# Performance work log

Hardware: AMD Instinct MI355X
Metric: run time of the kernel (lower is better)

Reference implementation:

```python
import jax, jax.numpy as jnp
import numpy as np

EPS = 1e-5


def setup_inputs() -> dict:
    key = jax.random.key(0)
    ks = jax.random.split(key, 8)
    g, p, d, h, w = 32, 64, 512, 24, 8
    hw = h * w
    return {
        "gal_fea": jax.random.normal(ks[0], (g, d, h, w), dtype=jnp.float32),
        "prob_fea": jax.random.normal(ks[1], (p, d, h, w), dtype=jnp.float32),
        "bn_weight": jnp.ones((1,), jnp.float32),
        "bn_bias": jnp.zeros((1,), jnp.float32),
        "bn_mean": jax.random.normal(ks[2], (1,), jnp.float32) * 0.1,
        "bn_var": jax.random.uniform(ks[3], (1,), jnp.float32, 0.5, 1.5),
        "fc_weight": jax.random.normal(ks[4], (1, 2 * hw), jnp.float32) * 0.05,
        "fc_bias": jnp.zeros((1,), jnp.float32),
        "lbn_weight": jnp.ones((1,), jnp.float32),
        "lbn_bias": jnp.zeros((1,), jnp.float32),
        "lbn_mean": jax.random.normal(ks[5], (1,), jnp.float32) * 0.1,
        "lbn_var": jax.random.uniform(ks[6], (1,), jnp.float32, 0.5, 1.5),
    }


def reference(gal_fea, prob_fea, bn_weight, bn_bias, bn_mean, bn_var,
              fc_weight, fc_bias, lbn_weight, lbn_bias, lbn_mean, lbn_var):
    g, d, h, w = gal_fea.shape
    p = prob_fea.shape[0]
    hw = h * w
    # 1x1 conv with probe pixels as kernels == batched correlation (QK^T style)
    gal = gal_fea.reshape(g, d, hw)                                  # [g, d, hw_x]
    ker = jnp.transpose(prob_fea, (0, 2, 3, 1)).reshape(p, hw, d)    # [p, hw_y, d]
    s = jnp.einsum('gdx,pyd->gpyx', gal, ker)                        # [g, p, hw_y, hw_x]
    # dual-axis max pooling, then concat: [g, p, 2*hw]
    score = jnp.concatenate([s.max(axis=2), s.max(axis=3)], axis=-1)
    # BatchNorm1d(1) in eval mode: scalar affine with running stats
    score = (score - bn_mean) * (bn_weight / jnp.sqrt(bn_var + EPS)) + bn_bias
    # fc: Linear(2*hw, 1)
    score = score.reshape(g * p, 2 * hw) @ fc_weight[0] + fc_bias[0]  # [g*p]
    score = score.reshape(g, p)
    # logit BatchNorm1d(1), eval mode
    score = (score - lbn_mean) * (lbn_weight / jnp.sqrt(lbn_var + EPS)) + lbn_bias
    return jax.nn.sigmoid(score / 10.0)
```

## Files before the change

kernel.cpp:

```cpp
#include <hip/hip_runtime.h>
#include <hip/hip_bf16.h>
#include <cstdint>
#include <cstddef>

#define NG 32
#define NP 64
#define ND 512
#define HW 192
#define EPSV 1e-5f

typedef _Float16 half8 __attribute__((ext_vector_type(8)));
typedef float floatx4 __attribute__((ext_vector_type(4)));
typedef float floatx16 __attribute__((ext_vector_type(16)));

__global__ __launch_bounds__(192) void prep_probe(const float* __restrict__ prob,
                                                  _Float16* __restrict__ probT2) {
  const int p = blockIdx.x, s = blockIdx.y;
  const int r = threadIdx.x;
  const float* src = prob + ((size_t)p * ND + s * 8) * HW + r;
  half8 h;
#pragma unroll
  for (int j = 0; j < 8; ++j) h[j] = (_Float16)src[(size_t)j * HW];
  *(half8*)(probT2 + (((size_t)p * 64 + s) * HW + r) * 8) = h;
}

__global__ __launch_bounds__(256) void prep_gal(const float* __restrict__ gal,
                                                _Float16* __restrict__ galT) {
  __shared__ float tile[32][33];
  const int zg = blockIdx.z;
  const float* sp = gal + (size_t)zg * ND * HW;
  _Float16* dp = galT + (size_t)zg * HW * ND;
  const int k0 = blockIdx.x * 32, s0 = blockIdx.y * 32;
  const int tx = threadIdx.x & 31, ty = threadIdx.x >> 5;
#pragma unroll
  for (int i = ty; i < 32; i += 8)
    tile[i][tx] = sp[(size_t)(k0 + i) * HW + s0 + tx];
  __syncthreads();
#pragma unroll
  for (int i = ty; i < 32; i += 8)
    dp[(size_t)(s0 + i) * ND + k0 + tx] = (_Float16)tile[tx][i];
}

__device__ __forceinline__ void g2l16(const void* g, void* l) {
  __builtin_amdgcn_global_load_lds(
      (const __attribute__((address_space(1))) void*)g,
      (__attribute__((address_space(3))) void*)l, 16, 0, 0);
}

__global__ __launch_bounds__(256, 2) void qaconv_main(
    const _Float16* __restrict__ galT, const _Float16* __restrict__ probT2,
    const float* __restrict__ bn_w, const float* __restrict__ bn_b,
    const float* __restrict__ bn_m, const float* __restrict__ bn_v,
    const float* __restrict__ fc_w, const float* __restrict__ fc_b,
    const float* __restrict__ lbn_w, const float* __restrict__ lbn_b,
    const float* __restrict__ lbn_m, const float* __restrict__ lbn_v,
    float* __restrict__ out) {
  __shared__ __align__(16) char shmem[50688];
  __shared__ float colp[2][HW];
  __shared__ float wsum[4];
  char* bufB = shmem;
  float(*rowbuf)[66] = (float(*)[66])shmem;

  const int bid = blockIdx.x;
  const int g = bid >> 6, p = bid & 63;

  const int t = threadIdx.x;
  const int lane = t & 63, wid = t >> 6;
  const int wr = wid & 1;
  const int wc = wid >> 1;
  const int l31 = lane & 31, hi = lane >> 5;
  const int arow0 = wr * 96 + l31;

  const _Float16* aBase = probT2 + (((size_t)p * 64 + hi) * HW + arow0) * 8;

  const _Float16* gBl = galT + (size_t)g * HW * ND + (size_t)(t & 31) * ND + ((t >> 5) & 7) * 8;
  const int sdst = wid * 1024;

  floatx16 acc[3][3];
#pragma unroll
  for (int ii = 0; ii < 3; ++ii)
#pragma unroll
    for (int jj = 0; jj < 3; ++jj) acc[ii][jj] = (floatx16)0.f;

#define STAGE_B(kt_, buf_)                                          \
  {                                                                 \
    char* db_ = bufB + (buf_)*24576 + sdst;                         \
    const _Float16* sb_ = gBl + (size_t)(kt_)*64;                   \
    _Pragma("unroll") for (int r_ = 0; r_ < 6; ++r_)                \
        g2l16(sb_ + (size_t)r_ * 32 * ND, db_ + r_ * 4096);         \
  }

#define LOAD_AF(dst, idx_)                                          \
  {                                                                 \
    const _Float16* ap_ = aBase + (size_t)(idx_) * (2 * HW * 8);    \
    dst[0] = *(const half8*)(ap_);                                  \
    dst[1] = *(const half8*)(ap_ + 32 * 8);                         \
    dst[2] = *(const half8*)(ap_ + 64 * 8);                         \
  }

#define KC_BODY(kc_, AFU, AFL, nidx_)                                            \
  {                                                                              \
    LOAD_AF(AFL, nidx_);                                                         \
    half8 bf[3];                                                                 \
    const int boff_ = ((kc_)*2 + hi) * 512 + l31 * 16;                           \
    bf[0] = *(const half8*)(bcur + (wc * 3 + 0) * 4096 + boff_);                 \
    bf[1] = *(const half8*)(bcur + (wc * 3 + 1) * 4096 + boff_);                 \
    bf[2] = *(const half8*)(bcur + (wc * 3 + 2) * 4096 + boff_);                 \
    __builtin_amdgcn_s_setprio(1);                                               \
    _Pragma("unroll") for (int ii = 0; ii < 3; ++ii)                             \
        _Pragma("unroll") for (int jj = 0; jj < 3; ++jj)                         \
            acc[ii][jj] = __builtin_amdgcn_mfma_f32_32x32x16_f16(AFU[ii], bf[jj],\
                                                                 acc[ii][jj], 0, 0, 0); \
    __builtin_amdgcn_s_setprio(0);                                               \
  }

  half8 af0[3], af1[3];
  STAGE_B(0, 0);
  LOAD_AF(af0, 0);
  __syncthreads();

  for (int kt = 0; kt < 8; ++kt) {
    if (kt < 7) STAGE_B(kt + 1, (kt & 1) ^ 1);
    const char* bcur = bufB + (kt & 1) * 24576;
    const int i0 = kt * 4;
    const int n4 = (kt < 7) ? i0 + 4 : 31;
    KC_BODY(0, af0, af1, i0 + 1)
    KC_BODY(1, af1, af0, i0 + 2)
    KC_BODY(2, af0, af1, i0 + 3)
    KC_BODY(3, af1, af0, n4)
    __syncthreads();
  }

#pragma unroll
  for (int fb = 0; fb < 3; ++fb) {
    float v = -3.4e38f;
#pragma unroll
    for (int fa = 0; fa < 3; ++fa)
#pragma unroll
      for (int e = 0; e < 16; ++e) v = fmaxf(v, acc[fa][fb][e]);
    v = fmaxf(v, __shfl_xor(v, 32));
    if (lane < 32) colp[wr][wc * 96 + fb * 32 + lane] = v;
  }
#pragma unroll
  for (int fa = 0; fa < 3; ++fa)
#pragma unroll
    for (int e = 0; e < 16; ++e) {
      float rv = acc[fa][0][e];
      rv = fmaxf(rv, acc[fa][1][e]);
      rv = fmaxf(rv, acc[fa][2][e]);
      const int Y = wr * 96 + fa * 32 + (e & 3) + 8 * (e >> 2) + 4 * hi;
      rowbuf[Y][wc * 32 + l31] = rv;
    }
  __syncthreads();

  float partial = 0.f;
  if (t < HW) {
    const float* rb = rowbuf[t];
    float rmax = -3.4e38f;
#pragma unroll
    for (int j = 0; j < 16; ++j) {
      const floatx4 v = *(const floatx4*)&rb[j * 4];
      rmax = fmaxf(rmax, fmaxf(fmaxf(v[0], v[1]), fmaxf(v[2], v[3])));
    }
    const float cmax = fmaxf(colp[0][t], colp[1][t]);
    const float scale = bn_w[0] / sqrtf(bn_v[0] + EPSV);
    const float bm = bn_m[0], bb = bn_b[0];
    partial = ((cmax - bm) * scale + bb) * fc_w[t] +
              ((rmax - bm) * scale + bb) * fc_w[HW + t];
  }
#pragma unroll
  for (int off = 1; off < 64; off <<= 1) partial += __shfl_xor(partial, off);
  if (lane == 0) wsum[wid] = partial;
  __syncthreads();
  if (t == 0) {
    const float sum = fc_b[0] + wsum[0] + wsum[1] + wsum[2] + wsum[3];
    const float logit = (sum - lbn_m[0]) * (lbn_w[0] / sqrtf(lbn_v[0] + EPSV)) + lbn_b[0];
    out[bid] = 1.f / (1.f + expf(-logit * 0.1f));
  }
#undef STAGE_B
#undef LOAD_AF
#undef KC_BODY
}

__global__ __launch_bounds__(256) void qaconv_naive(
    const float* __restrict__ gal, const float* __restrict__ prob,
    const float* __restrict__ bn_w, const float* __restrict__ bn_b,
    const float* __restrict__ bn_m, const float* __restrict__ bn_v,
    const float* __restrict__ fc_w, const float* __restrict__ fc_b,
    const float* __restrict__ lbn_w, const float* __restrict__ lbn_b,
    const float* __restrict__ lbn_m, const float* __restrict__ lbn_v,
    float* __restrict__ out) {
  __shared__ float prow[ND];
  __shared__ float rowmaxs[HW];
  __shared__ float colmaxs[HW];
  __shared__ float red[4];
  const int bid = blockIdx.x;
  const int g = bid >> 6, p = bid & 63;
  const int t = threadIdx.x, lane = t & 63, wid = t >> 6;
  const float* gp = gal + (size_t)g * ND * HW;
  const float* pp = prob + (size_t)p * ND * HW;
  float colmax = -3.4e38f;
  for (int y = 0; y < HW; ++y) {
    for (int k = t; k < ND; k += 256) prow[k] = pp[(size_t)k * HW + y];
    __syncthreads();
    float sv = -3.4e38f;
    if (t < HW) {
      sv = 0.f;
      for (int k = 0; k < ND; ++k) sv = fmaf(prow[k], gp[(size_t)k * HW + t], sv);
      colmax = fmaxf(colmax, sv);
    }
    float m = sv;
#pragma unroll
    for (int off = 1; off < 64; off <<= 1) m = fmaxf(m, __shfl_xor(m, off));
    if (lane == 0) red[wid] = m;
    __syncthreads();
    if (t == 0) rowmaxs[y] = fmaxf(fmaxf(red[0], red[1]), fmaxf(red[2], red[3]));
    __syncthreads();
  }
  if (t < HW) colmaxs[t] = colmax;
  __syncthreads();
  float partial = 0.f;
  for (int j = t; j < 2 * HW; j += 256) {
    const float v = (j < HW) ? colmaxs[j] : rowmaxs[j - HW];
    const float sc = (v - bn_m[0]) * (bn_w[0] / sqrtf(bn_v[0] + EPSV)) + bn_b[0];
    partial += sc * fc_w[j];
  }
#pragma unroll
  for (int off = 1; off < 64; off <<= 1) partial += __shfl_xor(partial, off);
  if (lane == 0) red[wid] = partial;
  __syncthreads();
  if (t == 0) {
    const float sum = fc_b[0] + red[0] + red[1] + red[2] + red[3];
    const float logit = (sum - lbn_m[0]) * (lbn_w[0] / sqrtf(lbn_v[0] + EPSV)) + lbn_b[0];
    out[bid] = 1.f / (1.f + expf(-logit * 0.1f));
  }
}

extern "C" void kernel_launch(void* const* d_in, const int* in_sizes, int n_in,
                              void* d_out, int out_size, void* d_ws, size_t ws_size,
                              hipStream_t stream) {
  const float* gal = (const float*)d_in[0];
  const float* prob = (const float*)d_in[1];
  const float* bn_w = (const float*)d_in[2];
  const float* bn_b = (const float*)d_in[3];
  const float* bn_m = (const float*)d_in[4];
  const float* bn_v = (const float*)d_in[5];
  const float* fc_w = (const float*)d_in[6];
  const float* fc_b = (const float*)d_in[7];
  const float* lbn_w = (const float*)d_in[8];
  const float* lbn_b = (const float*)d_in[9];
  const float* lbn_m = (const float*)d_in[10];
  const float* lbn_v = (const float*)d_in[11];
  float* out = (float*)d_out;

  const size_t probT2_elems = (size_t)NP * 64 * HW * 8;
  const size_t galT_elems = (size_t)NG * HW * ND;
  const size_t ws_needed = (probT2_elems + galT_elems) * sizeof(_Float16);
  if (ws_size >= ws_needed) {
    _Float16* probT2 = (_Float16*)d_ws;
    _Float16* galT = probT2 + probT2_elems;
    prep_probe<<<dim3(NP, 64), dim3(192), 0, stream>>>(prob, probT2);
    prep_gal<<<dim3(16, 6, NG), dim3(256), 0, stream>>>(gal, galT);
    qaconv_main<<<dim3(NG * NP), dim3(256), 0, stream>>>(
        galT, probT2, bn_w, bn_b, bn_m, bn_v, fc_w, fc_b, lbn_w, lbn_b, lbn_m, lbn_v, out);
  } else {
    qaconv_naive<<<dim3(NG * NP), dim3(256), 0, stream>>>(
        gal, prob, bn_w, bn_b, bn_m, bn_v, fc_w, fc_b, lbn_w, lbn_b, lbn_m, lbn_v, out);
  }
}
```

Baseline: 108.5 us.

## Pre-tile both operands in MFMA fragment order and stage both through LDS

```diff
diff --git a/kernel.cpp b/kernel.cpp
--- a/kernel.cpp
+++ b/kernel.cpp
@@ -7,38 +7,41 @@
 #define NP 64
 #define ND 512
 #define HW 192
+#define KT2 16
 #define EPSV 1e-5f
 
 typedef _Float16 half8 __attribute__((ext_vector_type(8)));
 typedef float floatx4 __attribute__((ext_vector_type(4)));
 typedef float floatx16 __attribute__((ext_vector_type(16)));
 
-__global__ __launch_bounds__(192) void prep_probe(const float* __restrict__ prob,
-                                                  _Float16* __restrict__ probT2) {
-  const int p = blockIdx.x, s = blockIdx.y;
-  const int r = threadIdx.x;
-  const float* src = prob + ((size_t)p * ND + s * 8) * HW + r;
-  half8 h;
-#pragma unroll
-  for (int j = 0; j < 8; ++j) h[j] = (_Float16)src[(size_t)j * HW];
-  *(half8*)(probT2 + (((size_t)p * 64 + s) * HW + r) * 8) = h;
-}
-
-__global__ __launch_bounds__(256) void prep_gal(const float* __restrict__ gal,
-                                                _Float16* __restrict__ galT) {
-  __shared__ float tile[32][33];
-  const int zg = blockIdx.z;
-  const float* sp = gal + (size_t)zg * ND * HW;
-  _Float16* dp = galT + (size_t)zg * HW * ND;
-  const int k0 = blockIdx.x * 32, s0 = blockIdx.y * 32;
-  const int tx = threadIdx.x & 31, ty = threadIdx.x >> 5;
-#pragma unroll
-  for (int i = ty; i < 32; i += 8)
-    tile[i][tx] = sp[(size_t)(k0 + i) * HW + s0 + tx];
-  __syncthreads();
-#pragma unroll
-  for (int i = ty; i < 32; i += 8)
-    dp[(size_t)(s0 + i) * ND + k0 + tx] = (_Float16)tile[tx][i];
+__global__ __launch_bounds__(256) void prep_tiles(const float* __restrict__ gal,
+                                                  const float* __restrict__ prob,
+                                                  _Float16* __restrict__ galT3,
+                                                  _Float16* __restrict__ probT3) {
+  const int z = blockIdx.x;
+  const int kt2 = blockIdx.y;
+  const float* src;
+  _Float16* dst;
+  if (z < NP) {
+    src = prob + (size_t)z * ND * HW;
+    dst = probT3 + (size_t)z * KT2 * 6144;
+  } else {
+    src = gal + (size_t)(z - NP) * ND * HW;
+    dst = galT3 + (size_t)(z - NP) * KT2 * 6144;
+  }
+  src += (size_t)kt2 * 32 * HW;
+  dst += (size_t)kt2 * 6144;
+  const int t = threadIdx.x;
+#pragma unroll
+  for (int r = 0; r < 3; ++r) {
+    const int h = r * 256 + t;
+    const int rb = h >> 7, kc = (h >> 6) & 1, hi = (h >> 5) & 1, l31 = h & 31;
+    const float* sp = src + (size_t)(kc * 16 + hi * 8) * HW + rb * 32 + l31;
+    half8 v;
+#pragma unroll
+    for (int j = 0; j < 8; ++j) v[j] = (_Float16)sp[(size_t)j * HW];
+    *(half8*)(dst + (size_t)h * 8) = v;
+  }
 }
 
 __device__ __forceinline__ void g2l16(const void* g, void* l) {
@@ -48,7 +51,7 @@
 }
 
 __global__ __launch_bounds__(256, 2) void qaconv_main(
-    const _Float16* __restrict__ galT, const _Float16* __restrict__ probT2,
+    const _Float16* __restrict__ galT3, const _Float16* __restrict__ probT3,
     const float* __restrict__ bn_w, const float* __restrict__ bn_b,
     const float* __restrict__ bn_m, const float* __restrict__ bn_v,
     const float* __restrict__ fc_w, const float* __restrict__ fc_b,
@@ -58,7 +61,7 @@
   __shared__ __align__(16) char shmem[50688];
   __shared__ float colp[2][HW];
   __shared__ float wsum[4];
-  char* bufB = shmem;
+  char* bufs = shmem;
   float(*rowbuf)[66] = (float(*)[66])shmem;
 
   const int bid = blockIdx.x;
@@ -69,11 +72,9 @@
   const int wr = wid & 1;
   const int wc = wid >> 1;
   const int l31 = lane & 31, hi = lane >> 5;
-  const int arow0 = wr * 96 + l31;
-
-  const _Float16* aBase = probT2 + (((size_t)p * 64 + hi) * HW + arow0) * 8;
-
-  const _Float16* gBl = galT + (size_t)g * HW * ND + (size_t)(t & 31) * ND + ((t >> 5) & 7) * 8;
+
+  const _Float16* pAl = probT3 + (size_t)p * KT2 * 6144 + wid * 512 + lane * 8;
+  const _Float16* pBl = galT3 + (size_t)g * KT2 * 6144 + wid * 512 + lane * 8;
   const int sdst = wid * 1024;
 
   floatx16 acc[3][3];
@@ -82,52 +83,44 @@
 #pragma unroll
     for (int jj = 0; jj < 3; ++jj) acc[ii][jj] = (floatx16)0.f;
 
-#define STAGE_B(kt_, buf_)                                          \
-  {                                                                 \
-    char* db_ = bufB + (buf_)*24576 + sdst;                         \
-    const _Float16* sb_ = gBl + (size_t)(kt_)*64;                   \
-    _Pragma("unroll") for (int r_ = 0; r_ < 6; ++r_)                \
-        g2l16(sb_ + (size_t)r_ * 32 * ND, db_ + r_ * 4096);         \
-  }
-
-#define LOAD_AF(dst, idx_)                                          \
-  {                                                                 \
-    const _Float16* ap_ = aBase + (size_t)(idx_) * (2 * HW * 8);    \
-    dst[0] = *(const half8*)(ap_);                                  \
-    dst[1] = *(const half8*)(ap_ + 32 * 8);                         \
-    dst[2] = *(const half8*)(ap_ + 64 * 8);                         \
-  }
-
-#define KC_BODY(kc_, AFU, AFL, nidx_)                                            \
+#define STAGE(kt_, b_)                                               \
+  {                                                                  \
+    char* db_ = bufs + (b_)*24576 + sdst;                            \
+    const _Float16* sa_ = pAl + (size_t)(kt_)*6144;                  \
+    const _Float16* sb_ = pBl + (size_t)(kt_)*6144;                  \
+    _Pragma("unroll") for (int r_ = 0; r_ < 3; ++r_)                 \
+        g2l16(sa_ + (size_t)r_ * 2048, db_ + r_ * 4096);             \
+    _Pragma("unroll") for (int r_ = 0; r_ < 3; ++r_)                 \
+        g2l16(sb_ + (size_t)r_ * 2048, db_ + 12288 + r_ * 4096);     \
+  }
+
+#define KC_BODY(kc_)                                                             \
   {                                                                              \
-    LOAD_AF(AFL, nidx_);                                                         \
-    half8 bf[3];                                                                 \
-    const int boff_ = ((kc_)*2 + hi) * 512 + l31 * 16;                           \
-    bf[0] = *(const half8*)(bcur + (wc * 3 + 0) * 4096 + boff_);                 \
-    bf[1] = *(const half8*)(bcur + (wc * 3 + 1) * 4096 + boff_);                 \
-    bf[2] = *(const half8*)(bcur + (wc * 3 + 2) * 4096 + boff_);                 \
+    half8 af[3], bf[3];                                                          \
+    const int off_ = (kc_)*1024 + hi * 512 + l31 * 16;                           \
+    af[0] = *(const half8*)(bA + (wr * 3 + 0) * 2048 + off_);                    \
+    af[1] = *(const half8*)(bA + (wr * 3 + 1) * 2048 + off_);                    \
+    af[2] = *(const half8*)(bA + (wr * 3 + 2) * 2048 + off_);                    \
+    bf[0] = *(const half8*)(bB + (wc * 3 + 0) * 2048 + off_);                    \
+    bf[1] = *(const half8*)(bB + (wc * 3 + 1) * 2048 + off_);                    \
+    bf[2] = *(const half8*)(bB + (wc * 3 + 2) * 2048 + off_);                    \
     __builtin_amdgcn_s_setprio(1);                                               \
     _Pragma("unroll") for (int ii = 0; ii < 3; ++ii)                             \
         _Pragma("unroll") for (int jj = 0; jj < 3; ++jj)                         \
-            acc[ii][jj] = __builtin_amdgcn_mfma_f32_32x32x16_f16(AFU[ii], bf[jj],\
+            acc[ii][jj] = __builtin_amdgcn_mfma_f32_32x32x16_f16(af[ii], bf[jj], \
                                                                  acc[ii][jj], 0, 0, 0); \
     __builtin_amdgcn_s_setprio(0);                                               \
   }
 
-  half8 af0[3], af1[3];
-  STAGE_B(0, 0);
-  LOAD_AF(af0, 0);
-  __syncthreads();
-
-  for (int kt = 0; kt < 8; ++kt) {
-    if (kt < 7) STAGE_B(kt + 1, (kt & 1) ^ 1);
-    const char* bcur = bufB + (kt & 1) * 24576;
-    const int i0 = kt * 4;
-    const int n4 = (kt < 7) ? i0 + 4 : 31;
-    KC_BODY(0, af0, af1, i0 + 1)
-    KC_BODY(1, af1, af0, i0 + 2)
-    KC_BODY(2, af0, af1, i0 + 3)
-    KC_BODY(3, af1, af0, n4)
+  STAGE(0, 0);
+  __syncthreads();
+
+  for (int kt = 0; kt < KT2; ++kt) {
+    if (kt < KT2 - 1) STAGE(kt + 1, (kt & 1) ^ 1);
+    const char* bA = bufs + (kt & 1) * 24576;
+    const char* bB = bA + 12288;
+    KC_BODY(0)
+    KC_BODY(1)
     __syncthreads();
   }
 
@@ -177,8 +170,7 @@
     const float logit = (sum - lbn_m[0]) * (lbn_w[0] / sqrtf(lbn_v[0] + EPSV)) + lbn_b[0];
     out[bid] = 1.f / (1.f + expf(-logit * 0.1f));
   }
-#undef STAGE_B
-#undef LOAD_AF
+#undef STAGE
 #undef KC_BODY
 }
 
@@ -253,16 +245,15 @@
   const float* lbn_v = (const float*)d_in[11];
   float* out = (float*)d_out;
 
-  const size_t probT2_elems = (size_t)NP * 64 * HW * 8;
-  const size_t galT_elems = (size_t)NG * HW * ND;
-  const size_t ws_needed = (probT2_elems + galT_elems) * sizeof(_Float16);
+  const size_t probT3_elems = (size_t)NP * KT2 * 6144;
+  const size_t galT3_elems = (size_t)NG * KT2 * 6144;
+  const size_t ws_needed = (probT3_elems + galT3_elems) * sizeof(_Float16);
   if (ws_size >= ws_needed) {
-    _Float16* probT2 = (_Float16*)d_ws;
-    _Float16* galT = probT2 + probT2_elems;
-    prep_probe<<<dim3(NP, 64), dim3(192), 0, stream>>>(prob, probT2);
-    prep_gal<<<dim3(16, 6, NG), dim3(256), 0, stream>>>(gal, galT);
+    _Float16* probT3 = (_Float16*)d_ws;
+    _Float16* galT3 = probT3 + probT3_elems;
+    prep_tiles<<<dim3(NP + NG, KT2), dim3(256), 0, stream>>>(gal, prob, galT3, probT3);
     qaconv_main<<<dim3(NG * NP), dim3(256), 0, stream>>>(
-        galT, probT2, bn_w, bn_b, bn_m, bn_v, fc_w, fc_b, lbn_w, lbn_b, lbn_m, lbn_v, out);
+        galT3, probT3, bn_w, bn_b, bn_m, bn_v, fc_w, fc_b, lbn_w, lbn_b, lbn_m, lbn_v, out);
   } else {
     qaconv_naive<<<dim3(NG * NP), dim3(256), 0, stream>>>(
         gal, prob, bn_w, bn_b, bn_m, bn_v, fc_w, fc_b, lbn_w, lbn_b, lbn_m, lbn_v, out);
```

New measurement: 91.38 us. -15.8%, faster.
